# Optimization experiments

Hardware: AMD Instinct MI355X
Metric: run time of the kernel (lower is better)

Reference implementation:

```python
import jax, jax.numpy as jnp
import numpy as np

FEAT_IN = 64     # len(nonterminals)
EMB = 256        # embedding_dim
K = 30           # sortk
B = 48           # batch items
NG = 11          # graphs per item (1 goal + 10 env)
G = B * NG       # 528 graphs
NPG = 192        # nodes per graph
EPG = 384        # edges per graph
N = G * NPG
E = G * EPG
D = 3 * EMB + 1  # 769, concat channel dim = conv5 kernel/stride
DENSE = (K // 2 - 5 + 1) * EMB  # 11*256 = 2816


def setup_inputs() -> dict:
    key = jax.random.key(0)
    ks = jax.random.split(key, 12)
    x = jax.random.normal(ks[0], (N, FEAT_IN), jnp.float32)
    # edges within each graph, no self loops (remove_self_loops in original)
    src_l = jax.random.randint(ks[1], (E,), 0, NPG)
    off = jax.random.randint(ks[2], (E,), 1, NPG)
    dst_l = (src_l + off) % NPG
    goff = (jnp.arange(E) // EPG) * NPG
    src = (src_l + goff).astype(jnp.int32)
    dst = (dst_l + goff).astype(jnp.int32)

    def lin(k, fi, fo):
        return (jax.random.normal(k, (fi, fo), jnp.float32) / np.float32(np.sqrt(fi)))

    return dict(
        x=x, src=src, dst=dst,
        W1=lin(ks[3], FEAT_IN, EMB), b1=jnp.zeros((EMB,), jnp.float32),
        W2=lin(ks[4], EMB, EMB), b2=jnp.zeros((EMB,), jnp.float32),
        W3=lin(ks[5], EMB, EMB), b3=jnp.zeros((EMB,), jnp.float32),
        W4=lin(ks[6], EMB, 1), b4=jnp.zeros((1,), jnp.float32),
        w5=jax.random.normal(ks[7], (EMB // 2, 1, D), jnp.float32) / np.float32(np.sqrt(D)),
        bc5=jnp.zeros((EMB // 2,), jnp.float32),
        w6=jax.random.normal(ks[8], (EMB, EMB // 2, 5), jnp.float32) / np.float32(np.sqrt(5 * EMB // 2)),
        bc6=jnp.zeros((EMB,), jnp.float32),
        Wc1=lin(ks[9], NG * DENSE, EMB), bc1=jnp.zeros((EMB,), jnp.float32),
        Wc2=lin(ks[10], EMB, 10), bc2=jnp.zeros((10,), jnp.float32),
    )


def _gcn(x, W, b, src, dst):
    # PyG GCNConv: add self loops, symmetric norm D^-1/2 (A+I) D^-1/2 (XW) + b
    h = x @ W
    deg = jnp.ones((N,), h.dtype).at[dst].add(1.0)  # +1 for self loop
    dis = jax.lax.rsqrt(deg)
    msg = h[src] * (dis[src] * dis[dst])[:, None]
    agg = jnp.zeros_like(h).at[dst].add(msg)
    return agg + h * (dis * dis)[:, None] + b  # self-loop norm = 1/deg


def _conv1d(x, w, b, stride):
    y = jax.lax.conv_general_dilated(x, w, (stride,), 'VALID',
                                     dimension_numbers=('NCH', 'OIH', 'NCH'))
    return y + b[None, :, None]


def reference(x, src, dst, W1, b1, W2, b2, W3, b3, W4, b4,
              w5, bc5, w6, bc6, Wc1, bc1, Wc2, bc2):
    x1 = jnp.tanh(_gcn(x, W1, b1, src, dst))
    x2 = jnp.tanh(_gcn(x1, W2, b2, src, dst))
    x3 = jnp.tanh(_gcn(x2, W3, b3, src, dst))
    x4 = jnp.tanh(_gcn(x3, W4, b4, src, dst))
    xc = jnp.concatenate([x1, x2, x3, x4], axis=-1)  # [N, D]
    xg = xc.reshape(G, NPG, D)
    # global_sort_pool: sort nodes per graph by last channel (desc), take top K
    _, idx = jax.lax.top_k(xg[:, :, -1], K)          # [G, K]
    xs = jnp.take_along_axis(xg, idx[:, :, None], axis=1)  # [G, K, D]
    seq = xs.reshape(G, 1, K * D)
    y = jax.nn.relu(_conv1d(seq, w5, bc5, D))        # [G, EMB/2, K]
    y = y.reshape(G, EMB // 2, K // 2, 2).max(axis=-1)  # MaxPool1d(2,2)
    y = jax.nn.relu(_conv1d(y, w6, bc6, 1))          # [G, EMB, K//2-4]
    emb = y.reshape(B, NG * DENSE)                   # 11 graphs per item, flattened
    h = jax.nn.relu(emb @ Wc1 + bc1)
    logits = h @ Wc2 + bc2                           # dropout is identity at eval
    return logits
```

## Files before the change

### kernel.cpp

```cpp
#include <hip/hip_runtime.h>
#include <hip/hip_bf16.h>

#define EMB   256
#define KSORT 30
#define BATCH 48
#define NGPI  11
#define GG    528
#define NPG   192
#define EPG   384
#define DCH   769
#define GC    176
#define NCH   (GG/GC)
#define MC    (GC*NPG)
#define EC    (GC*EPG)
#define FQ    44
#define FCH   (2816/FQ)
#define KB5   5

__device__ __forceinline__ int clampi(int v, int lo, int hi) {
  return v < lo ? lo : (v > hi ? hi : v);
}

__device__ __attribute__((aligned(16))) float g_c1[MC * EMB];
__device__ __attribute__((aligned(16))) float g_c2[MC * EMB];
__device__ __attribute__((aligned(16))) float g_c3[MC * EMB];
__device__ __attribute__((aligned(16))) float g_tb[MC * EMB];
__device__ __attribute__((aligned(16))) float g_dis[MC];
__device__ __attribute__((aligned(16))) float g_x4[MC];
__device__ __attribute__((aligned(16))) int   g_indptr[MC + 1];
__device__ __attribute__((aligned(16))) int   g_ssrc[EC];
__device__ __attribute__((aligned(16))) int   g_idx[GC * KSORT];
__device__ __attribute__((aligned(16))) float g_w5t[DCH * 128];
__device__ __attribute__((aligned(16))) float g_w6t[640 * 256];
__device__ __attribute__((aligned(16))) float g_y[GC * 128 * 30];
__device__ __attribute__((aligned(16))) float g_y2[GC * 128 * 15];
__device__ __attribute__((aligned(16))) float g_z[GG * 2816];
__device__ __attribute__((aligned(16))) float g_hp[NGPI * FQ * BATCH * 256];
__device__ __attribute__((aligned(16))) float g_h[BATCH * 256];

__device__ __forceinline__ float* selbuf(int s) {
  return s == 0 ? g_c1 : (s == 1 ? g_c2 : g_c3);
}

__global__ __launch_bounds__(192) void build_csr_k(const int* __restrict__ src,
    const int* __restrict__ dst, int g0) {
  __shared__ int cnt[NPG];
  __shared__ int offs[NPG];
  int g = blockIdx.x, t = threadIdx.x;
  int gg = g0 + g;
  cnt[t] = 0;
  __syncthreads();
  int ebase = gg * EPG, gnb = gg * NPG, lnb = g * NPG;
  for (int e = t; e < EPG; e += 192) {
    int dl = clampi(dst[ebase + e] - gnb, 0, NPG - 1);
    atomicAdd(&cnt[dl], 1);
  }
  __syncthreads();
  if (t == 0) {
    int run = g * EPG;
    for (int i = 0; i < NPG; i++) { offs[i] = run; run += cnt[i]; }
  }
  __syncthreads();
  g_indptr[lnb + t] = offs[t];
  g_dis[lnb + t] = 1.0f / sqrtf(1.0f + (float)cnt[t]);
  if (g == 0 && t == 0) g_indptr[MC] = EC;
  __syncthreads();
  for (int e = t; e < EPG; e += 192) {
    int ee = ebase + e;
    int dl = clampi(dst[ee] - gnb, 0, NPG - 1);
    int pos = clampi(atomicAdd(&offs[dl], 1), 0, EC - 1);
    g_ssrc[pos] = clampi(src[ee] - gnb, 0, NPG - 1) + lnb;
  }
}

template<bool AX>
__global__ __launch_bounds__(256) void gemm_k(const float* __restrict__ Ax,
    int asel, const float* __restrict__ W, int Kd, int mglob0) {
  __shared__ float As[16][68];
  __shared__ float Bs[16][68];
  const int m0 = blockIdx.x * 64, n0 = blockIdx.y * 64;
  const int t = threadIdx.x;
  const int tx = t & 15, ty = t >> 4;
  float acc[4][4];
#pragma unroll
  for (int i = 0; i < 4; i++)
#pragma unroll
    for (int j = 0; j < 4; j++) acc[i][j] = 0.f;
  const int arow = t >> 2, akk = (t & 3) * 4;
  const int bkk = t >> 4, bn = (t & 15) * 4;
  const float* Ap = AX ? (Ax + (size_t)mglob0 * Kd) : selbuf(asel);
  for (int k0 = 0; k0 < Kd; k0 += 16) {
    {
      const float* p = Ap + (size_t)(m0 + arow) * Kd + k0 + akk;
      float4 v = *(const float4*)p;
      As[akk + 0][arow] = v.x; As[akk + 1][arow] = v.y;
      As[akk + 2][arow] = v.z; As[akk + 3][arow] = v.w;
    }
    {
      const float* q = W + (size_t)(k0 + bkk) * EMB + n0 + bn;
      *(float4*)&Bs[bkk][bn] = *(const float4*)q;
    }
    __syncthreads();
#pragma unroll
    for (int kk = 0; kk < 16; kk++) {
      float a[4], b[4];
#pragma unroll
      for (int i = 0; i < 4; i++) a[i] = As[kk][ty * 4 + i];
#pragma unroll
      for (int j = 0; j < 4; j++) b[j] = Bs[kk][tx * 4 + j];
#pragma unroll
      for (int i = 0; i < 4; i++)
#pragma unroll
        for (int j = 0; j < 4; j++) acc[i][j] += a[i] * b[j];
    }
    __syncthreads();
  }
#pragma unroll
  for (int i = 0; i < 4; i++) {
    float* cp = g_tb + (size_t)(m0 + ty * 4 + i) * EMB + n0 + tx * 4;
    *(float4*)cp = make_float4(acc[i][0], acc[i][1], acc[i][2], acc[i][3]);
  }
}

__global__ __launch_bounds__(256) void agg_k(int osel, const float* __restrict__ bias) {
  int n = blockIdx.x * 4 + (threadIdx.x >> 6);
  int lane = threadIdx.x & 63;
  float dn = g_dis[n];
  const float4* H4 = (const float4*)g_tb;
  float4 hv = H4[(size_t)n * 64 + lane];
  float sc = dn * dn;
  float ax = hv.x * sc, ay = hv.y * sc, az = hv.z * sc, aw = hv.w * sc;
  int beg = g_indptr[n], end = g_indptr[n + 1];
  for (int j = beg; j < end; j++) {
    int s = g_ssrc[j];
    float c = g_dis[s] * dn;
    float4 v = H4[(size_t)s * 64 + lane];
    ax += v.x * c; ay += v.y * c; az += v.z * c; aw += v.w * c;
  }
  float4 bv = ((const float4*)bias)[lane];
  float4 o;
  o.x = tanhf(ax + bv.x);
  o.y = tanhf(ay + bv.y);
  o.z = tanhf(az + bv.z);
  o.w = tanhf(aw + bv.w);
  ((float4*)selbuf(osel))[(size_t)n * 64 + lane] = o;
}

__global__ __launch_bounds__(256) void gemm4_k(const float* __restrict__ W4) {
  int n = blockIdx.x * 4 + (threadIdx.x >> 6);
  int lane = threadIdx.x & 63;
  float4 a = *(const float4*)(g_c3 + (size_t)n * EMB + lane * 4);
  float4 w = *(const float4*)(W4 + lane * 4);
  float s = a.x * w.x + a.y * w.y + a.z * w.z + a.w * w.w;
  for (int off = 32; off > 0; off >>= 1) s += __shfl_down(s, off, 64);
  if (lane == 0) g_tb[n] = s;
}

__global__ __launch_bounds__(256) void agg4_k(const float* __restrict__ b4) {
  int n = blockIdx.x * 256 + threadIdx.x;
  if (n >= MC) return;
  float dn = g_dis[n];
  float acc = g_tb[n] * dn * dn;
  int beg = g_indptr[n], end = g_indptr[n + 1];
  for (int j = beg; j < end; j++) {
    int s = g_ssrc[j];
    acc += g_tb[s] * g_dis[s] * dn;
  }
  g_x4[n] = tanhf(acc + b4[0]);
}

__global__ __launch_bounds__(256) void sortpool_k() {
  __shared__ float sv[256];
  __shared__ int si[256];
  int g = blockIdx.x, t = threadIdx.x;
  if (t < NPG) { sv[t] = g_x4[g * NPG + t]; si[t] = t; }
  else { sv[t] = -1e30f; si[t] = 1 << 20; }
  __syncthreads();
  for (int k = 2; k <= 256; k <<= 1) {
    for (int j = k >> 1; j > 0; j >>= 1) {
      int ixj = t ^ j;
      if (ixj > t) {
        float v1 = sv[t], v2 = sv[ixj];
        int i1 = si[t], i2 = si[ixj];
        bool before_t = (v1 > v2) || (v1 == v2 && i1 < i2);
        bool up = ((t & k) == 0);
        if (up ? !before_t : before_t) {
          sv[t] = v2; sv[ixj] = v1;
          si[t] = i2; si[ixj] = i1;
        }
      }
      __syncthreads();
    }
  }
  if (t < KSORT) g_idx[g * KSORT + t] = clampi(g * NPG + si[t], 0, MC - 1);
}

__global__ __launch_bounds__(256) void tw5_k(const float* __restrict__ w5) {
  int i = blockIdx.x * 256 + threadIdx.x;
  if (i >= 128 * DCH) return;
  int o = i / DCH, d = i % DCH;
  g_w5t[d * 128 + o] = w5[i];
}
__global__ __launch_bounds__(256) void tw6_k(const float* __restrict__ w6) {
  int i = blockIdx.x * 256 + threadIdx.x;
  if (i >= 256 * 640) return;
  int o = i / 640, ir = i % 640;
  g_w6t[ir * 256 + o] = w6[i];
}

__global__ __launch_bounds__(128) void conv5_k(const float* __restrict__ bc5) {
  __shared__ float ar[KB5][772];
  int g = blockIdx.x, kb = blockIdx.y * KB5;
  int t = threadIdx.x;
  for (int kk = 0; kk < KB5; kk++) {
    int n = clampi(g_idx[g * KSORT + kb + kk], 0, MC - 1);
    const float* p1 = g_c1 + (size_t)n * EMB;
    const float* p2 = g_c2 + (size_t)n * EMB;
    const float* p3 = g_c3 + (size_t)n * EMB;
    for (int d = t; d < EMB; d += 128) {
      ar[kk][d] = p1[d];
      ar[kk][EMB + d] = p2[d];
      ar[kk][2 * EMB + d] = p3[d];
    }
    if (t == 0) ar[kk][768] = g_x4[n];
  }
  __syncthreads();
  float acc[KB5];
  float bias = bc5[t];
#pragma unroll
  for (int kk = 0; kk < KB5; kk++) acc[kk] = bias;
  const float* wbase = g_w5t + t;
  int d = 0;
  for (; d + 8 <= DCH; d += 8) {
    float w0 = wbase[(d + 0) * 128], w1 = wbase[(d + 1) * 128];
    float w2 = wbase[(d + 2) * 128], w3 = wbase[(d + 3) * 128];
    float w4 = wbase[(d + 4) * 128], w5 = wbase[(d + 5) * 128];
    float w6 = wbase[(d + 6) * 128], w7 = wbase[(d + 7) * 128];
#pragma unroll
    for (int kk = 0; kk < KB5; kk++) {
      float4 a0 = *(const float4*)&ar[kk][d];
      float4 a1 = *(const float4*)&ar[kk][d + 4];
      acc[kk] += a0.x * w0 + a0.y * w1 + a0.z * w2 + a0.w * w3 +
                 a1.x * w4 + a1.y * w5 + a1.z * w6 + a1.w * w7;
    }
  }
  for (; d < DCH; d++) {
    float wv = wbase[d * 128];
#pragma unroll
    for (int kk = 0; kk < KB5; kk++) acc[kk] += ar[kk][d] * wv;
  }
#pragma unroll
  for (int kk = 0; kk < KB5; kk++)
    g_y[(size_t)g * 3840 + t * KSORT + kb + kk] = fmaxf(acc[kk], 0.f);
}

__global__ void maxpool_k() {
  int i = blockIdx.x * 256 + threadIdx.x;
  if (i >= GC * 128 * 15) return;
  int j = i % 15, go = i / 15;
  g_y2[i] = fmaxf(g_y[go * 30 + 2 * j], g_y[go * 30 + 2 * j + 1]);
}

__global__ __launch_bounds__(256) void conv6_k(const float* __restrict__ bc6,
                                               int g0) {
  __shared__ float s[128 * 16];
  int g = blockIdx.x, t = threadIdx.x;
  for (int i = t; i < 1920; i += 256) {
    int ch = i / 15, j = i % 15;
    s[ch * 16 + j] = g_y2[(size_t)g * 1920 + i];
  }
  __syncthreads();
  float acc[11];
  float bias = bc6[t];
#pragma unroll
  for (int q = 0; q < 11; q++) acc[q] = bias;
  for (int i = 0; i < 128; i += 2) {
    float wA[5], wB[5];
#pragma unroll
    for (int r = 0; r < 5; r++) {
      wA[r] = g_w6t[(i * 5 + r) * 256 + t];
      wB[r] = g_w6t[((i + 1) * 5 + r) * 256 + t];
    }
    const float* sA = &s[i * 16];
    const float* sB = &s[(i + 1) * 16];
#pragma unroll
    for (int r = 0; r < 5; r++)
#pragma unroll
      for (int q = 0; q < 11; q++)
        acc[q] += sA[r + q] * wA[r] + sB[r + q] * wB[r];
  }
#pragma unroll
  for (int q = 0; q < 11; q++)
    g_z[(size_t)(g0 + g) * 2816 + t * 11 + q] = fmaxf(acc[q], 0.f);
}

__global__ __launch_bounds__(128) void dense1_k(const float* __restrict__ Wc1) {
  __shared__ float zs[BATCH][FCH];
  int gi = blockIdx.x;
  int obase = blockIdx.y * 128;
  int fq = blockIdx.z, f0 = fq * FCH;
  int t = threadIdx.x;
  for (int i = t; i < BATCH * FCH; i += 128) {
    int gl = i >> 6, f = i & 63;
    zs[gl][f] = g_z[(size_t)(gl * NGPI + gi) * 2816 + f0 + f];
  }
  __syncthreads();
  const float* wp = Wc1 + (size_t)gi * 2816 * 256 + (size_t)f0 * 256 + obase + t;
  float acc[BATCH];
#pragma unroll
  for (int gl = 0; gl < BATCH; gl++) acc[gl] = 0.f;
  float wc[8];
#pragma unroll
  for (int r = 0; r < 8; r++) wc[r] = wp[(size_t)r * 256];
  for (int f = 0; f < FCH; f += 8) {
    float wn[8];
    int fn = (f + 8 < FCH) ? f + 8 : f;
#pragma unroll
    for (int r = 0; r < 8; r++) wn[r] = wp[(size_t)(fn + r) * 256];
#pragma unroll
    for (int gl = 0; gl < BATCH; gl++) {
      float4 z0 = *(const float4*)&zs[gl][f];
      float4 z1 = *(const float4*)&zs[gl][f + 4];
      acc[gl] += z0.x * wc[0] + z0.y * wc[1] + z0.z * wc[2] + z0.w * wc[3] +
                 z1.x * wc[4] + z1.y * wc[5] + z1.z * wc[6] + z1.w * wc[7];
    }
#pragma unroll
    for (int r = 0; r < 8; r++) wc[r] = wn[r];
  }
  float* hp = g_hp + (size_t)(gi * FQ + fq) * (BATCH * 256);
#pragma unroll
  for (int gl = 0; gl < BATCH; gl++)
    hp[gl * 256 + obase + t] = acc[gl];
}

__global__ __launch_bounds__(256) void reduce_k() {
  int j = blockIdx.x * 256 + threadIdx.x;
  if (j >= BATCH * 256) return;
  float s0 = 0.f, s1 = 0.f, s2 = 0.f, s3 = 0.f;
  const size_t STR = BATCH * 256;
  for (int p = 0; p < NGPI * FQ; p += 4) {
    s0 += g_hp[(size_t)(p + 0) * STR + j];
    s1 += g_hp[(size_t)(p + 1) * STR + j];
    s2 += g_hp[(size_t)(p + 2) * STR + j];
    s3 += g_hp[(size_t)(p + 3) * STR + j];
  }
  g_h[j] = (s0 + s1) + (s2 + s3);
}

__global__ __launch_bounds__(256) void dense2_k(const float* __restrict__ bc1,
    const float* __restrict__ Wc2, const float* __restrict__ bc2,
    float* __restrict__ out) {
  __shared__ float hs[BATCH * 256];
  int t = threadIdx.x;
  for (int i = t; i < BATCH * 256; i += 256) {
    int o = i & 255;
    hs[i] = fmaxf(g_h[i] + bc1[o], 0.f);
  }
  __syncthreads();
  for (int i = t; i < 480; i += 256) {
    int b = i / 10, c = i % 10;
    float acc = bc2[c];
    for (int k = 0; k < 256; k++) acc += hs[b * 256 + k] * Wc2[k * 10 + c];
    out[i] = acc;
  }
}

__global__ void diag_k(float* __restrict__ out, float v) {
  int i = blockIdx.x * 256 + threadIdx.x;
  if (i < 480) out[i] = v;
}

extern "C" void kernel_launch(void* const* d_in, const int* in_sizes, int n_in,
                              void* d_out, int out_size, void* d_ws, size_t ws_size,
                              hipStream_t stream) {
  const float* x   = (const float*)d_in[0];
  const int*   src = (const int*)d_in[1];
  const int*   dst = (const int*)d_in[2];
  const float* W1  = (const float*)d_in[3];
  const float* b1  = (const float*)d_in[4];
  const float* W2  = (const float*)d_in[5];
  const float* b2  = (const float*)d_in[6];
  const float* W3  = (const float*)d_in[7];
  const float* b3  = (const float*)d_in[8];
  const float* W4  = (const float*)d_in[9];
  const float* b4  = (const float*)d_in[10];
  const float* w5  = (const float*)d_in[11];
  const float* bc5 = (const float*)d_in[12];
  const float* w6  = (const float*)d_in[13];
  const float* bc6 = (const float*)d_in[14];
  const float* Wc1 = (const float*)d_in[15];
  const float* bc1 = (const float*)d_in[16];
  const float* Wc2 = (const float*)d_in[17];
  const float* bc2 = (const float*)d_in[18];
  float* out = (float*)d_out;

  (void)hipGetLastError();
  int lcount = 0, fidx = -1;
  hipError_t ferr = hipSuccess;
  auto ck = [&]() {
    hipError_t e = hipGetLastError();
    if (e != hipSuccess && ferr == hipSuccess) { ferr = e; fidx = lcount; }
    lcount++;
  };

  tw5_k<<<(128 * DCH + 255) / 256, 256, 0, stream>>>(w5); ck();
  tw6_k<<<(256 * 640 + 255) / 256, 256, 0, stream>>>(w6); ck();

  dim3 gg(MC / 64, 4);
  for (int c = 0; c < NCH; c++) {
    const int g0 = c * GC, nbase = g0 * NPG;
    build_csr_k<<<GC, 192, 0, stream>>>(src, dst, g0); ck();
    gemm_k<true><<<gg, 256, 0, stream>>>(x, 0, W1, 64, nbase); ck();
    agg_k<<<MC / 4, 256, 0, stream>>>(0, b1); ck();
    gemm_k<false><<<gg, 256, 0, stream>>>(nullptr, 0, W2, EMB, 0); ck();
    agg_k<<<MC / 4, 256, 0, stream>>>(1, b2); ck();
    gemm_k<false><<<gg, 256, 0, stream>>>(nullptr, 1, W3, EMB, 0); ck();
    agg_k<<<MC / 4, 256, 0, stream>>>(2, b3); ck();
    gemm4_k<<<MC / 4, 256, 0, stream>>>(W4); ck();
    agg4_k<<<MC / 256, 256, 0, stream>>>(b4); ck();
    sortpool_k<<<GC, 256, 0, stream>>>(); ck();
    conv5_k<<<dim3(GC, 6), 128, 0, stream>>>(bc5); ck();
    maxpool_k<<<(GC * 1920 + 255) / 256, 256, 0, stream>>>(); ck();
    conv6_k<<<GC, 256, 0, stream>>>(bc6, g0); ck();
  }

  dense1_k<<<dim3(NGPI, 2, FQ), 128, 0, stream>>>(Wc1); ck();
  reduce_k<<<(BATCH * 256 + 255) / 256, 256, 0, stream>>>(); ck();
  dense2_k<<<1, 256, 0, stream>>>(bc1, Wc2, bc2, out); ck();

  if (ferr != hipSuccess) {
    int code = (int)ferr; if (code > 100) code = 100;
    float v = (fidx == 0) ? (1024.f + 8.f * code) : (2048.f + 16.f * code);
    diag_k<<<2, 256, 0, stream>>>(out, v);
  }
}
```

Measured before the change: 1.164 ms.

## Process all graphs in one pass and use larger register-tiled GEMM

Removes the three-chunk loop so every kernel launches once over all 528 graphs, which cuts launch count and gives each launch more parallelism. The device-global scratch buffers grow threefold to match. The GEMM moves from 64x64 tiles with 4x4 per thread to 128x128 tiles with 8x8 per thread, using vectorized shared-memory reads and register prefetch of the next K slice. This raises register pressure and may lower occupancy.

```diff
diff --git a/kernel.cpp b/kernel.cpp
--- a/kernel.cpp
+++ b/kernel.cpp
@@ -9,7 +9,7 @@
 #define NPG   192
 #define EPG   384
 #define DCH   769
-#define GC    176
+#define GC    528
 #define NCH   (GG/GC)
 #define MC    (GC*NPG)
 #define EC    (GC*EPG)
@@ -75,50 +75,62 @@
 
 template<bool AX>
 __global__ __launch_bounds__(256) void gemm_k(const float* __restrict__ Ax,
-    int asel, const float* __restrict__ W, int Kd, int mglob0) {
-  __shared__ float As[16][68];
-  __shared__ float Bs[16][68];
-  const int m0 = blockIdx.x * 64, n0 = blockIdx.y * 64;
+    int asel, const float* __restrict__ W, int Kd) {
+  __shared__ float As[16][132];
+  __shared__ float Bs[16][132];
+  const int m0 = blockIdx.x * 128, n0 = blockIdx.y * 128;
   const int t = threadIdx.x;
   const int tx = t & 15, ty = t >> 4;
-  float acc[4][4];
-#pragma unroll
-  for (int i = 0; i < 4; i++)
-#pragma unroll
-    for (int j = 0; j < 4; j++) acc[i][j] = 0.f;
-  const int arow = t >> 2, akk = (t & 3) * 4;
-  const int bkk = t >> 4, bn = (t & 15) * 4;
-  const float* Ap = AX ? (Ax + (size_t)mglob0 * Kd) : selbuf(asel);
-  for (int k0 = 0; k0 < Kd; k0 += 16) {
-    {
-      const float* p = Ap + (size_t)(m0 + arow) * Kd + k0 + akk;
-      float4 v = *(const float4*)p;
-      As[akk + 0][arow] = v.x; As[akk + 1][arow] = v.y;
-      As[akk + 2][arow] = v.z; As[akk + 3][arow] = v.w;
-    }
-    {
-      const float* q = W + (size_t)(k0 + bkk) * EMB + n0 + bn;
-      *(float4*)&Bs[bkk][bn] = *(const float4*)q;
-    }
+  const int arow = t >> 1, acol = (t & 1) * 8;
+  const int brow = t >> 4, bcol = (t & 15) * 8;
+  float acc[8][8];
+#pragma unroll
+  for (int i = 0; i < 8; i++)
+#pragma unroll
+    for (int j = 0; j < 8; j++) acc[i][j] = 0.f;
+  const float* Ap = AX ? Ax : selbuf(asel);
+  const float* arp = Ap + (size_t)(m0 + arow) * Kd + acol;
+  const float* brp = W + (size_t)brow * EMB + n0 + bcol;
+  const int nt = Kd >> 4;
+  float4 a0 = *(const float4*)(arp);
+  float4 a1 = *(const float4*)(arp + 4);
+  float4 b0 = *(const float4*)(brp);
+  float4 b1 = *(const float4*)(brp + 4);
+  for (int it = 0; it < nt; ++it) {
+    As[acol + 0][arow] = a0.x; As[acol + 1][arow] = a0.y;
+    As[acol + 2][arow] = a0.z; As[acol + 3][arow] = a0.w;
+    As[acol + 4][arow] = a1.x; As[acol + 5][arow] = a1.y;
+    As[acol + 6][arow] = a1.z; As[acol + 7][arow] = a1.w;
+    *(float4*)&Bs[brow][bcol] = b0;
+    *(float4*)&Bs[brow][bcol + 4] = b1;
     __syncthreads();
+    if (it + 1 < nt) {
+      const float* ap = arp + (it + 1) * 16;
+      const float* bp = brp + (size_t)(it + 1) * 16 * EMB;
+      a0 = *(const float4*)(ap);
+      a1 = *(const float4*)(ap + 4);
+      b0 = *(const float4*)(bp);
+      b1 = *(const float4*)(bp + 4);
+    }
 #pragma unroll
     for (int kk = 0; kk < 16; kk++) {
-      float a[4], b[4];
-#pragma unroll
-      for (int i = 0; i < 4; i++) a[i] = As[kk][ty * 4 + i];
-#pragma unroll
-      for (int j = 0; j < 4; j++) b[j] = Bs[kk][tx * 4 + j];
-#pragma unroll
-      for (int i = 0; i < 4; i++)
-#pragma unroll
-        for (int j = 0; j < 4; j++) acc[i][j] += a[i] * b[j];
+      float a[8], b[8];
+      *(float4*)&a[0] = *(const float4*)&As[kk][ty * 8];
+      *(float4*)&a[4] = *(const float4*)&As[kk][ty * 8 + 4];
+      *(float4*)&b[0] = *(const float4*)&Bs[kk][tx * 8];
+      *(float4*)&b[4] = *(const float4*)&Bs[kk][tx * 8 + 4];
+#pragma unroll
+      for (int i = 0; i < 8; i++)
+#pragma unroll
+        for (int j = 0; j < 8; j++) acc[i][j] += a[i] * b[j];
     }
     __syncthreads();
   }
 #pragma unroll
-  for (int i = 0; i < 4; i++) {
-    float* cp = g_tb + (size_t)(m0 + ty * 4 + i) * EMB + n0 + tx * 4;
+  for (int i = 0; i < 8; i++) {
+    float* cp = g_tb + (size_t)(m0 + ty * 8 + i) * EMB + n0 + tx * 8;
     *(float4*)cp = make_float4(acc[i][0], acc[i][1], acc[i][2], acc[i][3]);
+    *(float4*)(cp + 4) = make_float4(acc[i][4], acc[i][5], acc[i][6], acc[i][7]);
   }
 }
 
@@ -406,23 +418,20 @@
   tw5_k<<<(128 * DCH + 255) / 256, 256, 0, stream>>>(w5); ck();
   tw6_k<<<(256 * 640 + 255) / 256, 256, 0, stream>>>(w6); ck();
 
-  dim3 gg(MC / 64, 4);
-  for (int c = 0; c < NCH; c++) {
-    const int g0 = c * GC, nbase = g0 * NPG;
-    build_csr_k<<<GC, 192, 0, stream>>>(src, dst, g0); ck();
-    gemm_k<true><<<gg, 256, 0, stream>>>(x, 0, W1, 64, nbase); ck();
-    agg_k<<<MC / 4, 256, 0, stream>>>(0, b1); ck();
-    gemm_k<false><<<gg, 256, 0, stream>>>(nullptr, 0, W2, EMB, 0); ck();
-    agg_k<<<MC / 4, 256, 0, stream>>>(1, b2); ck();
-    gemm_k<false><<<gg, 256, 0, stream>>>(nullptr, 1, W3, EMB, 0); ck();
-    agg_k<<<MC / 4, 256, 0, stream>>>(2, b3); ck();
-    gemm4_k<<<MC / 4, 256, 0, stream>>>(W4); ck();
-    agg4_k<<<MC / 256, 256, 0, stream>>>(b4); ck();
-    sortpool_k<<<GC, 256, 0, stream>>>(); ck();
-    conv5_k<<<dim3(GC, 6), 128, 0, stream>>>(bc5); ck();
-    maxpool_k<<<(GC * 1920 + 255) / 256, 256, 0, stream>>>(); ck();
-    conv6_k<<<GC, 256, 0, stream>>>(bc6, g0); ck();
-  }
+  dim3 gg(MC / 128, 2);
+  build_csr_k<<<GC, 192, 0, stream>>>(src, dst, 0); ck();
+  gemm_k<true><<<gg, 256, 0, stream>>>(x, 0, W1, 64); ck();
+  agg_k<<<MC / 4, 256, 0, stream>>>(0, b1); ck();
+  gemm_k<false><<<gg, 256, 0, stream>>>(nullptr, 0, W2, EMB); ck();
+  agg_k<<<MC / 4, 256, 0, stream>>>(1, b2); ck();
+  gemm_k<false><<<gg, 256, 0, stream>>>(nullptr, 1, W3, EMB); ck();
+  agg_k<<<MC / 4, 256, 0, stream>>>(2, b3); ck();
+  gemm4_k<<<MC / 4, 256, 0, stream>>>(W4); ck();
+  agg4_k<<<MC / 256, 256, 0, stream>>>(b4); ck();
+  sortpool_k<<<GC, 256, 0, stream>>>(); ck();
+  conv5_k<<<dim3(GC, 6), 128, 0, stream>>>(bc5); ck();
+  maxpool_k<<<(GC * 1920 + 255) / 256, 256, 0, stream>>>(); ck();
+  conv6_k<<<GC, 256, 0, stream>>>(bc6, 0); ck();
 
   dense1_k<<<dim3(NGPI, 2, FQ), 128, 0, stream>>>(Wc1); ck();
   reduce_k<<<(BATCH * 256 + 255) / 256, 256, 0, stream>>>(); ck();
```

After: 982.7 us. 15.6% less time.
